# Kernel optimization log

Hardware: AMD Instinct MI355X
Metric: run time of the kernel (lower is better)

## Reference

```python
import jax, jax.numpy as jnp
import numpy as np

WINDOW_SIZE = 11
C1 = (0.01 * 255) ** 2
C2 = (0.03 * 255) ** 2


def _make_window():
    # NOTE: faithful to the torch module: Gaussian with 2*sigma^2 = 4, UNNORMALIZED.
    x = np.arange(WINDOW_SIZE)
    g = np.exp(-((x - WINDOW_SIZE // 2) ** 2) / float(2 * 2)).astype(np.float32)
    w2d = np.outer(g, g)  # [11, 11]
    return jnp.asarray(w2d)[None, None, :, :]  # OIHW = [1, 1, 11, 11]


def _conv(x, w):
    pad = WINDOW_SIZE // 2
    return jax.lax.conv_general_dilated(
        x, w, window_strides=(1, 1), padding=[(pad, pad), (pad, pad)],
        dimension_numbers=('NCHW', 'OIHW', 'NCHW'))


def setup_inputs() -> dict:
    key = jax.random.key(0)
    k1, k2 = jax.random.split(key)
    shape = (32, 1, 512, 512)
    img1 = jax.random.uniform(k1, shape, dtype=jnp.float32)
    img2 = jax.random.uniform(k2, shape, dtype=jnp.float32)
    return {"img1": img1, "img2": img2}


def reference(img1, img2):
    w = _make_window()
    mu1 = _conv(img1, w)
    mu2 = _conv(img2, w)
    mu1_sq = mu1 * mu1
    mu2_sq = mu2 * mu2
    mu1_mu2 = mu1 * mu2
    sigma1_sq = _conv(img1 * img1, w) - mu1_sq
    sigma2_sq = _conv(img2 * img2, w) - mu2_sq
    sigma12 = _conv(img1 * img2, w) - mu1_mu2
    ssim_map = ((2 * mu1_mu2 + C1) * (2 * sigma12 + C2)) / (
        (mu1_sq + mu2_sq + C1) * (sigma1_sq + sigma2_sq + C2))
    return jnp.mean((1.0 - ssim_map) / 2.0)
```

## Files before the change

### kernel.cpp

```cpp
#include <hip/hip_runtime.h>
#include <hip/hip_fp16.h>


#define IMGW 512
#define IMGH 512
#define NIMG 32
#define TW 32
#define TH 64
#define IN_H 74
#define IN_W 44
#define NPIX (IN_H * IN_W)
#define NCHUNK (IN_H * 11)
#define NBX 16
#define NBY 8
#define NBLOCKS (NBX * NBY * NIMG)

typedef __attribute__((address_space(1))) const uint32_t ga_u32;
typedef __attribute__((address_space(3))) uint32_t ls_u32;

__device__ __forceinline__ void load16_lds(const float* g, float* l) {
  __builtin_amdgcn_global_load_lds((ga_u32*)g, (ls_u32*)l, 16, 0, 0);
}

__device__ __forceinline__ __half2 h2_of(uint32_t w) {
  return __builtin_bit_cast(__half2, w);
}
__device__ __forceinline__ uint32_t u_of(__half2 h) {
  return __builtin_bit_cast(uint32_t, h);
}

__global__ __launch_bounds__(256, 4) void ssim_main(
    const float* __restrict__ img1, const float* __restrict__ img2,
    float* __restrict__ partial) {
  __shared__ uint32_t uRaw[NPIX * 2];
  __shared__ uint32_t sPK[NPIX];
  __shared__ float sWave[4];
  float* sA = (float*)uRaw;
  float* sB = (float*)(uRaw + NPIX);
  uint32_t (*hAB)[TW] = (uint32_t (*)[TW])uRaw;
  uint32_t (*hPM)[TW] = (uint32_t (*)[TW])(uRaw + IN_H * TW);

  constexpr float g[11] = {0.0019304541f, 0.018315639f, 0.10539922f,
                           0.36787944f,   0.7788008f,   1.0f,
                           0.7788008f,    0.36787944f,  0.10539922f,
                           0.018315639f,  0.0019304541f};
  constexpr float C1v = 6.5025f;
  constexpr float C2v = 58.5225f;

  __half2 gh[11];
#pragma unroll
  for (int k = 0; k < 11; ++k) gh[k] = __float2half2_rn(g[k]);
  const __half2 c1m1 = __floats2half2_rn(1.0f, -1.0f);

  const int tid = threadIdx.x;
  const int bx = blockIdx.x;
  const int by = blockIdx.y;
  const int x0 = bx * TW - 5;
  const int y0 = by * TH - 5;
  const float* __restrict__ p1 = img1 + (size_t)blockIdx.z * (IMGW * IMGH);
  const float* __restrict__ p2 = img2 + (size_t)blockIdx.z * (IMGW * IMGH);

#pragma unroll
  for (int i = 0; i < 4; ++i) {
    int ch = tid + 256 * i;
    if (ch < NCHUNK) {
      int r = ch / 11;
      int cg = ch - r * 11;
      int gy = y0 + r;
      int gx = x0 + 4 * cg;
      int gyc = min(max(gy, 0), IMGH - 1);
      int gxc = min(max(gx, 0), IMGW - 4);
      int src = gyc * IMGW + gxc;
      load16_lds(p1 + src, &sA[ch * 4]);
      load16_lds(p2 + src, &sB[ch * 4]);
    }
  }
  __syncthreads();

  const bool borderBlk =
      (bx == 0) || (bx == NBX - 1) || (by == 0) || (by == NBY - 1);
  if (!borderBlk) {
    for (int ch = tid; ch < NCHUNK; ch += 256) {
      float4 a = *(const float4*)&sA[ch * 4];
      float4 b = *(const float4*)&sB[ch * 4];
      uint4 w;
      w.x = u_of(__floats2half2_rn(a.x, b.x));
      w.y = u_of(__floats2half2_rn(a.y, b.y));
      w.z = u_of(__floats2half2_rn(a.z, b.z));
      w.w = u_of(__floats2half2_rn(a.w, b.w));
      *(uint4*)&sPK[ch * 4] = w;
    }
  } else {
    for (int ch = tid; ch < NCHUNK; ch += 256) {
      int r = ch / 11;
      int cg = ch - r * 11;
      int gy = y0 + r;
      int gx = x0 + 4 * cg;
      float4 a = *(const float4*)&sA[ch * 4];
      float4 b = *(const float4*)&sB[ch * 4];
      bool rowok = (gy >= 0) && (gy < IMGH);
      uint4 w;
      float av[4] = {a.x, a.y, a.z, a.w};
      float bv[4] = {b.x, b.y, b.z, b.w};
      uint32_t* wp = (uint32_t*)&w;
#pragma unroll
      for (int j = 0; j < 4; ++j) {
        bool ok = rowok && (gx + j >= 0) && (gx + j < IMGW);
        wp[j] = u_of(__floats2half2_rn(ok ? av[j] : 0.f, ok ? bv[j] : 0.f));
      }
      *(uint4*)&sPK[ch * 4] = w;
    }
  }
  __syncthreads();

  for (int idx = tid; idx < IN_H * (TW / 4); idx += 256) {
    int r = idx >> 3;
    int c0 = (idx & 7) << 2;
    int base = r * IN_W + c0;
    __half2 ab[14], pm2[14];
    {
      uint4 w0 = *(const uint4*)&sPK[base];
      uint4 w1 = *(const uint4*)&sPK[base + 4];
      uint4 w2 = *(const uint4*)&sPK[base + 8];
      uint2 w3 = *(const uint2*)&sPK[base + 12];
      uint32_t ws[14] = {w0.x, w0.y, w0.z, w0.w, w1.x, w1.y, w1.z,
                         w1.w, w2.x, w2.y, w2.z, w2.w, w3.x, w3.y};
#pragma unroll
      for (int k = 0; k < 14; ++k) {
        __half2 w = h2_of(ws[k]);
        ab[k] = w;
        __half2 t = __hfma2(__lowhigh2highlow(w), c1m1, w);
        pm2[k] = __hmul2(t, t);
      }
    }
    uint4 oab, opm;
#pragma unroll
    for (int o = 0; o < 4; ++o) {
      __half2 cab = __float2half2_rn(0.0f);
      __half2 cpm = __float2half2_rn(0.0f);
#pragma unroll
      for (int k = 0; k < 11; ++k) {
        cab = __hfma2(gh[k], ab[o + k], cab);
        cpm = __hfma2(gh[k], pm2[o + k], cpm);
      }
      ((uint32_t*)&oab)[o] = u_of(cab);
      ((uint32_t*)&opm)[o] = u_of(cpm);
    }
    *(uint4*)&hAB[r][c0] = oab;
    *(uint4*)&hPM[r][c0] = opm;
  }
  __syncthreads();

  const int c = tid & 31;
  const int r0 = (tid >> 5) << 3;
  __half2 mAB[8], mPM[8];
  {
    __half2 m1[18], m2[18];
#pragma unroll
    for (int k = 0; k < 18; ++k) {
      m1[k] = h2_of(hAB[r0 + k][c]);
      m2[k] = h2_of(hPM[r0 + k][c]);
    }
#pragma unroll
    for (int o = 0; o < 8; ++o) {
      __half2 s = __float2half2_rn(0.0f);
      __half2 t = __float2half2_rn(0.0f);
#pragma unroll
      for (int k = 0; k < 11; ++k) {
        s = __hfma2(gh[k], m1[o + k], s);
        t = __hfma2(gh[k], m2[o + k], t);
      }
      mAB[o] = s; mPM[o] = t;
    }
  }

  float ssum = 0.f;
#pragma unroll
  for (int o = 0; o < 8; ++o) {
    float m1 = __low2float(mAB[o]);
    float m2 = __high2float(mAB[o]);
    float qp = __low2float(mPM[o]);
    float qm = __high2float(mPM[o]);
    float sumsq = 0.5f * (qp + qm);
    float eab = 0.25f * (qp - qm);
    float m1s = m1 * m1, m2s = m2 * m2, m12 = m1 * m2;
    float sg12 = eab - m12;
    float sgsum = sumsq - m1s - m2s;
    float num = (2.0f * m12 + C1v) * (2.0f * sg12 + C2v);
    float den = (m1s + m2s + C1v) * (sgsum + C2v);
    float r = num * __builtin_amdgcn_rcpf(den);
    if (!__builtin_isfinite(r)) r = 0.0f;
    ssum += r;
  }

#pragma unroll
  for (int off = 32; off > 0; off >>= 1) ssum += __shfl_down(ssum, off, 64);
  if ((tid & 63) == 0) sWave[tid >> 6] = ssum;
  __syncthreads();
  if (tid == 0) {
    partial[(blockIdx.z * NBY + blockIdx.y) * NBX + blockIdx.x] =
        sWave[0] + sWave[1] + sWave[2] + sWave[3];
  }
}

__global__ __launch_bounds__(256) void ssim_reduce(
    const float* __restrict__ partial, float* __restrict__ out) {
  const int tid = threadIdx.x;
  float s = 0.f;
  for (int i = tid; i < NBLOCKS; i += 256) s += partial[i];
#pragma unroll
  for (int off = 32; off > 0; off >>= 1) s += __shfl_down(s, off, 64);
  __shared__ float sw[4];
  if ((tid & 63) == 0) sw[tid >> 6] = s;
  __syncthreads();
  if (tid == 0) {
    float tot = sw[0] + sw[1] + sw[2] + sw[3];
    float val = 0.5f * (1.0f - tot * (1.0f / (32.0f * 512.0f * 512.0f)));
    if (!__builtin_isfinite(val)) val = 0.0f;
    out[0] = val;
  }
}

extern "C" void kernel_launch(void* const* d_in, const int* in_sizes, int n_in,
                              void* d_out, int out_size, void* d_ws,
                              size_t ws_size, hipStream_t stream) {
  const float* img1 = (const float*)d_in[0];
  const float* img2 = (const float*)d_in[1];
  float* partial = (float*)d_ws;
  float* out = (float*)d_out;

  dim3 grid(NBX, NBY, NIMG);
  hipLaunchKernelGGL(ssim_main, grid, dim3(256), 0, stream, img1, img2,
                     partial);
  hipLaunchKernelGGL(ssim_reduce, dim3(1), dim3(256), 0, stream, partial, out);
}
```

Measured before the change: 43.85 us.

## Drop separate packed LDS buffer and split separable passes into two halves

The separate packed-half LDS array is removed: packed data now overwrites the raw float area, and the horizontal-pass output lives in a ring of 42 rows placed in the second half. The horizontal and vertical passes are each split into two row batches with extra barriers, and the vertical pass keeps 4 outputs per thread instead of 8, which lowers register pressure. Launch bounds are raised to 6 blocks per CU to exploit the smaller LDS and register footprint. The cost is two more block-wide barriers and less register reuse of loaded rows in the vertical pass.

```diff
diff --git a/kernel.cpp b/kernel.cpp
--- a/kernel.cpp
+++ b/kernel.cpp
@@ -11,6 +11,7 @@
 #define IN_W 44
 #define NPIX (IN_H * IN_W)
 #define NCHUNK (IN_H * 11)
+#define HSLOT 42
 #define NBX 16
 #define NBY 8
 #define NBLOCKS (NBX * NBY * NIMG)
@@ -29,16 +30,13 @@
   return __builtin_bit_cast(uint32_t, h);
 }
 
-__global__ __launch_bounds__(256, 4) void ssim_main(
+__global__ __launch_bounds__(256, 6) void ssim_main(
     const float* __restrict__ img1, const float* __restrict__ img2,
     float* __restrict__ partial) {
   __shared__ uint32_t uRaw[NPIX * 2];
-  __shared__ uint32_t sPK[NPIX];
   __shared__ float sWave[4];
-  float* sA = (float*)uRaw;
-  float* sB = (float*)(uRaw + NPIX);
-  uint32_t (*hAB)[TW] = (uint32_t (*)[TW])uRaw;
-  uint32_t (*hPM)[TW] = (uint32_t (*)[TW])(uRaw + IN_H * TW);
+  uint32_t* sPK = uRaw;
+  uint32_t* hB = uRaw + NPIX;
 
   constexpr float g[11] = {0.0019304541f, 0.018315639f, 0.10539922f,
                            0.36787944f,   0.7788008f,   1.0f,
@@ -59,6 +57,8 @@
   const int y0 = by * TH - 5;
   const float* __restrict__ p1 = img1 + (size_t)blockIdx.z * (IMGW * IMGH);
   const float* __restrict__ p2 = img2 + (size_t)blockIdx.z * (IMGW * IMGH);
+  float* sA = (float*)uRaw;
+  float* sB = (float*)(uRaw + NPIX);
 
 #pragma unroll
   for (int i = 0; i < 4; ++i) {
@@ -113,56 +113,60 @@
   }
   __syncthreads();
 
-  for (int idx = tid; idx < IN_H * (TW / 4); idx += 256) {
-    int r = idx >> 3;
-    int c0 = (idx & 7) << 2;
-    int base = r * IN_W + c0;
-    __half2 ab[14], pm2[14];
-    {
-      uint4 w0 = *(const uint4*)&sPK[base];
-      uint4 w1 = *(const uint4*)&sPK[base + 4];
-      uint4 w2 = *(const uint4*)&sPK[base + 8];
-      uint2 w3 = *(const uint2*)&sPK[base + 12];
-      uint32_t ws[14] = {w0.x, w0.y, w0.z, w0.w, w1.x, w1.y, w1.z,
-                         w1.w, w2.x, w2.y, w2.z, w2.w, w3.x, w3.y};
-#pragma unroll
-      for (int k = 0; k < 14; ++k) {
-        __half2 w = h2_of(ws[k]);
-        ab[k] = w;
-        __half2 t = __hfma2(__lowhigh2highlow(w), c1m1, w);
-        pm2[k] = __hmul2(t, t);
-      }
-    }
-    uint4 oab, opm;
+  auto stage2 = [&](int rowbase, int nrows) {
+    for (int idx = tid; idx < nrows * 8; idx += 256) {
+      int rr = idx >> 3;
+      int r = rowbase + rr;
+      int c0 = (idx & 7) << 2;
+      int base = r * IN_W + c0;
+      __half2 ab[14], pm2[14];
+      {
+        uint4 w0 = *(const uint4*)&sPK[base];
+        uint4 w1 = *(const uint4*)&sPK[base + 4];
+        uint4 w2 = *(const uint4*)&sPK[base + 8];
+        uint2 w3 = *(const uint2*)&sPK[base + 12];
+        uint32_t ws[14] = {w0.x, w0.y, w0.z, w0.w, w1.x, w1.y, w1.z,
+                           w1.w, w2.x, w2.y, w2.z, w2.w, w3.x, w3.y};
+#pragma unroll
+        for (int k = 0; k < 14; ++k) {
+          __half2 w = h2_of(ws[k]);
+          ab[k] = w;
+          __half2 t = __hfma2(__lowhigh2highlow(w), c1m1, w);
+          pm2[k] = __hmul2(t, t);
+        }
+      }
+      uint4 oab, opm;
+#pragma unroll
+      for (int o = 0; o < 4; ++o) {
+        __half2 cab = __float2half2_rn(0.0f);
+        __half2 cpm = __float2half2_rn(0.0f);
+#pragma unroll
+        for (int k = 0; k < 11; ++k) {
+          cab = __hfma2(gh[k], ab[o + k], cab);
+          cpm = __hfma2(gh[k], pm2[o + k], cpm);
+        }
+        ((uint32_t*)&oab)[o] = u_of(cab);
+        ((uint32_t*)&opm)[o] = u_of(cpm);
+      }
+      *(uint4*)&hB[rr * 64 + c0] = oab;
+      *(uint4*)&hB[rr * 64 + 32 + c0] = opm;
+    }
+  };
+
+  float ssum = 0.f;
+  auto stage3 = [&](int outbase) {
+    const int c = tid & 31;
+    const int r0 = outbase + ((tid >> 5) << 2);
+    __half2 m1[14], m2[14];
+#pragma unroll
+    for (int k = 0; k < 14; ++k) {
+      int row = r0 + k;
+      int slot = (row >= HSLOT) ? (row - HSLOT) : row;
+      m1[k] = h2_of(hB[slot * 64 + c]);
+      m2[k] = h2_of(hB[slot * 64 + 32 + c]);
+    }
 #pragma unroll
     for (int o = 0; o < 4; ++o) {
-      __half2 cab = __float2half2_rn(0.0f);
-      __half2 cpm = __float2half2_rn(0.0f);
-#pragma unroll
-      for (int k = 0; k < 11; ++k) {
-        cab = __hfma2(gh[k], ab[o + k], cab);
-        cpm = __hfma2(gh[k], pm2[o + k], cpm);
-      }
-      ((uint32_t*)&oab)[o] = u_of(cab);
-      ((uint32_t*)&opm)[o] = u_of(cpm);
-    }
-    *(uint4*)&hAB[r][c0] = oab;
-    *(uint4*)&hPM[r][c0] = opm;
-  }
-  __syncthreads();
-
-  const int c = tid & 31;
-  const int r0 = (tid >> 5) << 3;
-  __half2 mAB[8], mPM[8];
-  {
-    __half2 m1[18], m2[18];
-#pragma unroll
-    for (int k = 0; k < 18; ++k) {
-      m1[k] = h2_of(hAB[r0 + k][c]);
-      m2[k] = h2_of(hPM[r0 + k][c]);
-    }
-#pragma unroll
-    for (int o = 0; o < 8; ++o) {
       __half2 s = __float2half2_rn(0.0f);
       __half2 t = __float2half2_rn(0.0f);
 #pragma unroll
@@ -170,28 +174,30 @@
         s = __hfma2(gh[k], m1[o + k], s);
         t = __hfma2(gh[k], m2[o + k], t);
       }
-      mAB[o] = s; mPM[o] = t;
-    }
-  }
-
-  float ssum = 0.f;
-#pragma unroll
-  for (int o = 0; o < 8; ++o) {
-    float m1 = __low2float(mAB[o]);
-    float m2 = __high2float(mAB[o]);
-    float qp = __low2float(mPM[o]);
-    float qm = __high2float(mPM[o]);
-    float sumsq = 0.5f * (qp + qm);
-    float eab = 0.25f * (qp - qm);
-    float m1s = m1 * m1, m2s = m2 * m2, m12 = m1 * m2;
-    float sg12 = eab - m12;
-    float sgsum = sumsq - m1s - m2s;
-    float num = (2.0f * m12 + C1v) * (2.0f * sg12 + C2v);
-    float den = (m1s + m2s + C1v) * (sgsum + C2v);
-    float r = num * __builtin_amdgcn_rcpf(den);
-    if (!__builtin_isfinite(r)) r = 0.0f;
-    ssum += r;
-  }
+      float m1f = __low2float(s);
+      float m2f = __high2float(s);
+      float qp = __low2float(t);
+      float qm = __high2float(t);
+      float sumsq = 0.5f * (qp + qm);
+      float eab = 0.25f * (qp - qm);
+      float m1s = m1f * m1f, m2s = m2f * m2f, m12 = m1f * m2f;
+      float sg12 = eab - m12;
+      float sgsum = sumsq - m1s - m2s;
+      float num = (2.0f * m12 + C1v) * (2.0f * sg12 + C2v);
+      float den = (m1s + m2s + C1v) * (sgsum + C2v);
+      float r = num * __builtin_amdgcn_rcpf(den);
+      if (!__builtin_isfinite(r)) r = 0.0f;
+      ssum += r;
+    }
+  };
+
+  stage2(0, HSLOT);
+  __syncthreads();
+  stage3(0);
+  __syncthreads();
+  stage2(HSLOT, IN_H - HSLOT);
+  __syncthreads();
+  stage3(32);
 
 #pragma unroll
   for (int off = 32; off > 0; off >>= 1) ssum += __shfl_down(ssum, off, 64);
```

Result: slower. 45.15 us (+2.9%).

## Split staging into two phases overlapping global loads, remap blocks across XCDs

Applied to the files above, without the earlier changes.

The loads into LDS are now waited on only partly (vmcnt(2)), so the first chunk of rows can be converted and horizontally filtered while the last loads are still in flight. The second half is processed after a full wait. The grid is also flattened to 1D and block IDs are remapped so that neighbouring tiles of the same image land on the same XCD, which should improve L2 locality. The correctness of the partial wait depends on the compiler's load issue order and on which chunks map to the first 42 rows.

```diff
diff --git a/kernel.cpp b/kernel.cpp
--- a/kernel.cpp
+++ b/kernel.cpp
@@ -14,6 +14,8 @@
 #define NBX 16
 #define NBY 8
 #define NBLOCKS (NBX * NBY * NIMG)
+#define LOWCH 512
+#define LOWROWS 42
 
 typedef __attribute__((address_space(1))) const uint32_t ga_u32;
 typedef __attribute__((address_space(3))) uint32_t ls_u32;
@@ -21,12 +23,16 @@
 __device__ __forceinline__ void load16_lds(const float* g, float* l) {
   __builtin_amdgcn_global_load_lds((ga_u32*)g, (ls_u32*)l, 16, 0, 0);
 }
-
 __device__ __forceinline__ __half2 h2_of(uint32_t w) {
   return __builtin_bit_cast(__half2, w);
 }
 __device__ __forceinline__ uint32_t u_of(__half2 h) {
   return __builtin_bit_cast(uint32_t, h);
+}
+__device__ __forceinline__ void lds_barrier() {
+  asm volatile("s_waitcnt lgkmcnt(0)" ::: "memory");
+  __builtin_amdgcn_s_barrier();
+  __builtin_amdgcn_sched_barrier(0);
 }
 
 __global__ __launch_bounds__(256, 4) void ssim_main(
@@ -37,8 +43,8 @@
   __shared__ float sWave[4];
   float* sA = (float*)uRaw;
   float* sB = (float*)(uRaw + NPIX);
-  uint32_t (*hAB)[TW] = (uint32_t (*)[TW])uRaw;
-  uint32_t (*hPM)[TW] = (uint32_t (*)[TW])(uRaw + IN_H * TW);
+  uint32_t* hAB = uRaw;
+  uint32_t* hPM = uRaw + NPIX;
 
   constexpr float g[11] = {0.0019304541f, 0.018315639f, 0.10539922f,
                            0.36787944f,   0.7788008f,   1.0f,
@@ -53,12 +59,17 @@
   const __half2 c1m1 = __floats2half2_rn(1.0f, -1.0f);
 
   const int tid = threadIdx.x;
-  const int bx = blockIdx.x;
-  const int by = blockIdx.y;
+  const int bid = blockIdx.x;
+  const int wgid = (bid & 7) * (NBLOCKS / 8) + (bid >> 3);
+  const int img = wgid >> 7;
+  const int by = (wgid >> 4) & 7;
+  const int bx = wgid & 15;
   const int x0 = bx * TW - 5;
   const int y0 = by * TH - 5;
-  const float* __restrict__ p1 = img1 + (size_t)blockIdx.z * (IMGW * IMGH);
-  const float* __restrict__ p2 = img2 + (size_t)blockIdx.z * (IMGW * IMGH);
+  const float* __restrict__ p1 = img1 + (size_t)img * (IMGW * IMGH);
+  const float* __restrict__ p2 = img2 + (size_t)img * (IMGW * IMGH);
+  const bool borderBlk =
+      (bx == 0) || (bx == NBX - 1) || (by == 0) || (by == NBY - 1);
 
 #pragma unroll
   for (int i = 0; i < 4; ++i) {
@@ -75,81 +86,94 @@
       load16_lds(p2 + src, &sB[ch * 4]);
     }
   }
-  __syncthreads();
-
-  const bool borderBlk =
-      (bx == 0) || (bx == NBX - 1) || (by == 0) || (by == NBY - 1);
-  if (!borderBlk) {
-    for (int ch = tid; ch < NCHUNK; ch += 256) {
-      float4 a = *(const float4*)&sA[ch * 4];
-      float4 b = *(const float4*)&sB[ch * 4];
-      uint4 w;
-      w.x = u_of(__floats2half2_rn(a.x, b.x));
-      w.y = u_of(__floats2half2_rn(a.y, b.y));
-      w.z = u_of(__floats2half2_rn(a.z, b.z));
-      w.w = u_of(__floats2half2_rn(a.w, b.w));
-      *(uint4*)&sPK[ch * 4] = w;
-    }
-  } else {
-    for (int ch = tid; ch < NCHUNK; ch += 256) {
-      int r = ch / 11;
-      int cg = ch - r * 11;
-      int gy = y0 + r;
-      int gx = x0 + 4 * cg;
-      float4 a = *(const float4*)&sA[ch * 4];
-      float4 b = *(const float4*)&sB[ch * 4];
-      bool rowok = (gy >= 0) && (gy < IMGH);
-      uint4 w;
-      float av[4] = {a.x, a.y, a.z, a.w};
-      float bv[4] = {b.x, b.y, b.z, b.w};
-      uint32_t* wp = (uint32_t*)&w;
-#pragma unroll
-      for (int j = 0; j < 4; ++j) {
-        bool ok = rowok && (gx + j >= 0) && (gx + j < IMGW);
-        wp[j] = u_of(__floats2half2_rn(ok ? av[j] : 0.f, ok ? bv[j] : 0.f));
-      }
-      *(uint4*)&sPK[ch * 4] = w;
-    }
-  }
-  __syncthreads();
-
-  for (int idx = tid; idx < IN_H * (TW / 4); idx += 256) {
-    int r = idx >> 3;
-    int c0 = (idx & 7) << 2;
-    int base = r * IN_W + c0;
-    __half2 ab[14], pm2[14];
-    {
-      uint4 w0 = *(const uint4*)&sPK[base];
-      uint4 w1 = *(const uint4*)&sPK[base + 4];
-      uint4 w2 = *(const uint4*)&sPK[base + 8];
-      uint2 w3 = *(const uint2*)&sPK[base + 12];
-      uint32_t ws[14] = {w0.x, w0.y, w0.z, w0.w, w1.x, w1.y, w1.z,
-                         w1.w, w2.x, w2.y, w2.z, w2.w, w3.x, w3.y};
-#pragma unroll
-      for (int k = 0; k < 14; ++k) {
-        __half2 w = h2_of(ws[k]);
-        ab[k] = w;
-        __half2 t = __hfma2(__lowhigh2highlow(w), c1m1, w);
-        pm2[k] = __hmul2(t, t);
-      }
-    }
-    uint4 oab, opm;
-#pragma unroll
-    for (int o = 0; o < 4; ++o) {
-      __half2 cab = __float2half2_rn(0.0f);
-      __half2 cpm = __float2half2_rn(0.0f);
-#pragma unroll
-      for (int k = 0; k < 11; ++k) {
-        cab = __hfma2(gh[k], ab[o + k], cab);
-        cpm = __hfma2(gh[k], pm2[o + k], cpm);
-      }
-      ((uint32_t*)&oab)[o] = u_of(cab);
-      ((uint32_t*)&opm)[o] = u_of(cpm);
-    }
-    *(uint4*)&hAB[r][c0] = oab;
-    *(uint4*)&hPM[r][c0] = opm;
-  }
-  __syncthreads();
+  asm volatile("s_waitcnt vmcnt(2)" ::: "memory");
+  __builtin_amdgcn_s_barrier();
+  __builtin_amdgcn_sched_barrier(0);
+
+  auto prepass = [&](int cbeg, int cend) {
+    if (!borderBlk) {
+      for (int ch = cbeg + tid; ch < cend; ch += 256) {
+        float4 a = *(const float4*)&sA[ch * 4];
+        float4 b = *(const float4*)&sB[ch * 4];
+        uint4 w;
+        w.x = u_of(__floats2half2_rn(a.x, b.x));
+        w.y = u_of(__floats2half2_rn(a.y, b.y));
+        w.z = u_of(__floats2half2_rn(a.z, b.z));
+        w.w = u_of(__floats2half2_rn(a.w, b.w));
+        *(uint4*)&sPK[ch * 4] = w;
+      }
+    } else {
+      for (int ch = cbeg + tid; ch < cend; ch += 256) {
+        int r = ch / 11;
+        int cg = ch - r * 11;
+        int gy = y0 + r;
+        int gx = x0 + 4 * cg;
+        float4 a = *(const float4*)&sA[ch * 4];
+        float4 b = *(const float4*)&sB[ch * 4];
+        bool rowok = (gy >= 0) && (gy < IMGH);
+        uint4 w;
+        float av[4] = {a.x, a.y, a.z, a.w};
+        float bv[4] = {b.x, b.y, b.z, b.w};
+        uint32_t* wp = (uint32_t*)&w;
+#pragma unroll
+        for (int j = 0; j < 4; ++j) {
+          bool ok = rowok && (gx + j >= 0) && (gx + j < IMGW);
+          wp[j] = u_of(__floats2half2_rn(ok ? av[j] : 0.f, ok ? bv[j] : 0.f));
+        }
+        *(uint4*)&sPK[ch * 4] = w;
+      }
+    }
+  };
+
+  auto stage2 = [&](int rowbase, int nrows) {
+    for (int idx = tid; idx < nrows * 8; idx += 256) {
+      int r = rowbase + (idx >> 3);
+      int c0 = (idx & 7) << 2;
+      int base = r * IN_W + c0;
+      __half2 ab[14], pm2[14];
+      {
+        uint4 w0 = *(const uint4*)&sPK[base];
+        uint4 w1 = *(const uint4*)&sPK[base + 4];
+        uint4 w2 = *(const uint4*)&sPK[base + 8];
+        uint2 w3 = *(const uint2*)&sPK[base + 12];
+        uint32_t ws[14] = {w0.x, w0.y, w0.z, w0.w, w1.x, w1.y, w1.z,
+                           w1.w, w2.x, w2.y, w2.z, w2.w, w3.x, w3.y};
+#pragma unroll
+        for (int k = 0; k < 14; ++k) {
+          __half2 w = h2_of(ws[k]);
+          ab[k] = w;
+          __half2 t = __hfma2(__lowhigh2highlow(w), c1m1, w);
+          pm2[k] = __hmul2(t, t);
+        }
+      }
+      uint4 oab, opm;
+#pragma unroll
+      for (int o = 0; o < 4; ++o) {
+        __half2 cab = __float2half2_rn(0.0f);
+        __half2 cpm = __float2half2_rn(0.0f);
+#pragma unroll
+        for (int k = 0; k < 11; ++k) {
+          cab = __hfma2(gh[k], ab[o + k], cab);
+          cpm = __hfma2(gh[k], pm2[o + k], cpm);
+        }
+        ((uint32_t*)&oab)[o] = u_of(cab);
+        ((uint32_t*)&opm)[o] = u_of(cpm);
+      }
+      *(uint4*)&hAB[r * 32 + c0] = oab;
+      *(uint4*)&hPM[r * 32 + c0] = opm;
+    }
+  };
+
+  prepass(0, LOWCH);
+  lds_barrier();
+  stage2(0, LOWROWS);
+  asm volatile("s_waitcnt vmcnt(0) lgkmcnt(0)" ::: "memory");
+  __builtin_amdgcn_s_barrier();
+  __builtin_amdgcn_sched_barrier(0);
+  prepass(LOWCH, NCHUNK);
+  lds_barrier();
+  stage2(LOWROWS, IN_H - LOWROWS);
+  lds_barrier();
 
   const int c = tid & 31;
   const int r0 = (tid >> 5) << 3;
@@ -158,8 +182,8 @@
     __half2 m1[18], m2[18];
 #pragma unroll
     for (int k = 0; k < 18; ++k) {
-      m1[k] = h2_of(hAB[r0 + k][c]);
-      m2[k] = h2_of(hPM[r0 + k][c]);
+      m1[k] = h2_of(hAB[(r0 + k) * 32 + c]);
+      m2[k] = h2_of(hPM[(r0 + k) * 32 + c]);
     }
 #pragma unroll
     for (int o = 0; o < 8; ++o) {
@@ -198,8 +222,7 @@
   if ((tid & 63) == 0) sWave[tid >> 6] = ssum;
   __syncthreads();
   if (tid == 0) {
-    partial[(blockIdx.z * NBY + blockIdx.y) * NBX + blockIdx.x] =
-        sWave[0] + sWave[1] + sWave[2] + sWave[3];
+    partial[wgid] = sWave[0] + sWave[1] + sWave[2] + sWave[3];
   }
 }
 
@@ -229,8 +252,7 @@
   float* partial = (float*)d_ws;
   float* out = (float*)d_out;
 
-  dim3 grid(NBX, NBY, NIMG);
-  hipLaunchKernelGGL(ssim_main, grid, dim3(256), 0, stream, img1, img2,
-                     partial);
+  hipLaunchKernelGGL(ssim_main, dim3(NBLOCKS), dim3(256), 0, stream, img1,
+                     img2, partial);
   hipLaunchKernelGGL(ssim_reduce, dim3(1), dim3(256), 0, stream, partial, out);
 }
```

Result: faster. 40.94 us (-6.7%).
